# Kernel optimization log

Measured on AMD Instinct MI355X. Metric: run time of the kernel, lower is better.

Reference implementation:

```python
import jax, jax.numpy as jnp
import numpy as np

NUM_CLASSES = 2
THRESHOLD = 0.35   # overlap_thresh
NEG_POS = 7        # negative:positive mining ratio
VAR0, VAR1 = 0.1, 0.2  # self.variance


def point_form(boxes):
    # (cx,cy,w,h) -> (xmin,ymin,xmax,ymax); boxes [P,4]
    return jnp.concatenate([boxes[:, :2] - boxes[:, 2:] / 2,
                            boxes[:, :2] + boxes[:, 2:] / 2], axis=1)


def jaccard(box_a, box_b):
    # box_a [B,O,4] xyxy, box_b [P,4] xyxy -> IoU [B,O,P]
    max_xy = jnp.minimum(box_a[:, :, None, 2:], box_b[None, None, :, 2:])
    min_xy = jnp.maximum(box_a[:, :, None, :2], box_b[None, None, :, :2])
    wh = jnp.clip(max_xy - min_xy, 0.0)
    inter = wh[..., 0] * wh[..., 1]
    area_a = ((box_a[..., 2] - box_a[..., 0]) * (box_a[..., 3] - box_a[..., 1]))[:, :, None]
    area_b = ((box_b[:, 2] - box_b[:, 0]) * (box_b[:, 3] - box_b[:, 1]))[None, None, :]
    return inter / (area_a + area_b - inter)


def encode(matched, priors):
    # matched [B,P,4] xyxy, priors [1,P,4] cxcywh -> offsets [B,P,4]
    g_cxcy = (matched[..., :2] + matched[..., 2:]) / 2 - priors[..., :2]
    g_cxcy = g_cxcy / (VAR0 * priors[..., 2:])
    g_wh = (matched[..., 2:] - matched[..., :2]) / priors[..., 2:]
    g_wh = jnp.log(g_wh) / VAR1
    return jnp.concatenate([g_cxcy, g_wh], axis=-1)


def match(truths, labels, priors):
    # truths [B,O,4] xyxy, labels [B,O] float, priors [P,4] cxcywh
    overlaps = jaccard(truths, point_form(priors))      # [B,O,P]
    best_prior_idx = jnp.argmax(overlaps, axis=2)       # [B,O] best prior per gt
    best_truth_overlap = jnp.max(overlaps, axis=1)      # [B,P]
    best_truth_idx = jnp.argmax(overlaps, axis=1)       # [B,P] best gt per prior
    O = truths.shape[1]

    def fix(bto, bti, bpi):
        # ensure every gt keeps its best prior (index_fill_ / loop in torch)
        bto = bto.at[bpi].set(2.0)
        bti = bti.at[bpi].set(jnp.arange(O))
        return bto, bti

    best_truth_overlap, best_truth_idx = jax.vmap(fix)(
        best_truth_overlap, best_truth_idx, best_prior_idx)
    matched = jnp.take_along_axis(truths, best_truth_idx[..., None], axis=1)  # [B,P,4]
    conf = jnp.take_along_axis(labels, best_truth_idx, axis=1).astype(jnp.int32) + 1
    conf = jnp.where(best_truth_overlap < THRESHOLD, 0, conf)  # background
    loc = encode(matched, priors[None])
    return loc, conf


def setup_inputs() -> dict:
    key = jax.random.key(0)
    k1, k2, k3, k4, k5, k6 = jax.random.split(key, 6)
    B, P, O, C = 32, 32768, 32, NUM_CLASSES
    loc_data = jax.random.normal(k1, (B, P, 4), jnp.float32)
    conf_data = jax.random.normal(k2, (B, P, C), jnp.float32)
    # priors: (cx,cy,w,h) in [0,1], wh in [0.02,0.3]
    p_cxcy = jax.random.uniform(k3, (P, 2), jnp.float32)
    p_wh = 0.02 + 0.28 * jax.random.uniform(k4, (P, 2), jnp.float32)
    priors = jnp.concatenate([p_cxcy, p_wh], axis=1)
    # targets: valid xyxy boxes + label column (label 0 -> class 1 after +1)
    t_cxcy = 0.1 + 0.8 * jax.random.uniform(k5, (B, O, 2), jnp.float32)
    t_wh = 0.05 + 0.2 * jax.random.uniform(k6, (B, O, 2), jnp.float32)
    boxes = jnp.concatenate([t_cxcy - t_wh / 2, t_cxcy + t_wh / 2], axis=2)
    labels = jnp.zeros((B, O, 1), jnp.float32)
    targets = jnp.concatenate([boxes, labels], axis=2)
    return {"loc_data": loc_data, "conf_data": conf_data,
            "priors": priors, "targets": targets}


def reference(loc_data, conf_data, priors, targets):
    B, P, C = conf_data.shape
    truths = targets[..., :4]
    labels = targets[..., 4]
    loc_t, conf_t = match(truths, labels, priors)   # [B,P,4], [B,P] int
    pos = conf_t > 0                                # [B,P]

    # localization: smooth-L1 summed over positives
    diff = loc_data - loc_t
    ad = jnp.abs(diff)
    sl1 = jnp.where(ad < 1.0, 0.5 * diff * diff, ad - 0.5)
    loss_l = jnp.sum(sl1 * pos[..., None].astype(loc_data.dtype))

    # per-prior CE loss for hard-negative mining
    lse = jax.nn.logsumexp(conf_data, axis=2)                            # [B,P]
    picked = jnp.take_along_axis(conf_data, conf_t[..., None], axis=2)[..., 0]
    ce = lse - picked                                                    # [B,P]
    mine = jnp.where(pos, 0.0, ce)
    # double-argsort rank trick (descending)
    loss_idx = jnp.argsort(-mine, axis=1)
    idx_rank = jnp.argsort(loss_idx, axis=1)
    num_pos = jnp.sum(pos, axis=1, keepdims=True)                        # [B,1]
    num_neg = jnp.minimum(NEG_POS * num_pos, P - 1)
    neg = idx_rank < num_neg

    sel = pos | neg
    loss_c = jnp.sum(jnp.where(sel, ce, 0.0))

    N = jnp.maximum(jnp.sum(num_pos).astype(jnp.float32), 1.0)
    return loss_l / N, loss_c / N
```

## Files before the change

### kernel.cpp

```cpp
#include <hip/hip_runtime.h>
#include <stdint.h>

#define NB 32
#define NP 32768
#define NO 32
#define THRESH 0.35f

typedef unsigned long long u64;
typedef unsigned int u32;

__device__ __forceinline__ float iou_corners(float px1, float py1, float px2, float py2, float ab,
                                             float tx1, float ty1, float tx2, float ty2, float aa)
{
#pragma clang fp contract(off)
    float iw = fminf(tx2, px2) - fmaxf(tx1, px1);
    float ih = fminf(ty2, py2) - fmaxf(ty1, py1);
    iw = fmaxf(iw, 0.f); ih = fmaxf(ih, 0.f);
    float inter = iw * ih;
    return __fdividef(inter, aa + ab - inter);
}

__device__ __forceinline__ float smooth_l1_sum(float4 ld, float4 pr, float4 tt)
{
#pragma clang fp contract(off)
    float g0 = __fdividef((tt.x + tt.z) * 0.5f - pr.x, 0.1f * pr.z);
    float g1 = __fdividef((tt.y + tt.w) * 0.5f - pr.y, 0.1f * pr.w);
    float g2 = __logf(__fdividef(tt.z - tt.x, pr.z)) * 5.0f;
    float g3 = __logf(__fdividef(tt.w - tt.y, pr.w)) * 5.0f;
    float d0 = ld.x - g0, d1 = ld.y - g1, d2 = ld.z - g2, d3 = ld.w - g3;
    float a0 = fabsf(d0), a1 = fabsf(d1), a2 = fabsf(d2), a3 = fabsf(d3);
    return (a0 < 1.f ? 0.5f * d0 * d0 : a0 - 0.5f)
         + (a1 < 1.f ? 0.5f * d1 * d1 : a1 - 0.5f)
         + (a2 < 1.f ? 0.5f * d2 * d2 : a2 - 0.5f)
         + (a3 < 1.f ? 0.5f * d3 * d3 : a3 - 0.5f);
}

__device__ __forceinline__ float lse2(float c0, float c1)
{
#pragma clang fp contract(off)
    float mm = fmaxf(c0, c1), mn = fminf(c0, c1);
    return mm + __logf(1.f + __expf(mn - mm));
}

__global__ __launch_bounds__(256) void kern1(
        const float* __restrict__ loc, const float* __restrict__ conf,
        const float* __restrict__ priors, const float* __restrict__ targets,
        float* __restrict__ mine, u64* __restrict__ bpk_part,
        float* __restrict__ part_sl1, float* __restrict__ part_cep, int* __restrict__ part_np,
        float* __restrict__ sl_tot, float* __restrict__ c_tot,
        int* __restrict__ np_tot, int* __restrict__ done_cnt)
{
#pragma clang fp contract(off)
    __shared__ __align__(16) float4 tbc[NO];
    __shared__ float ta[NO], tlab[NO];
    __shared__ u64 keys[NO];
    __shared__ float rs0[4], rs1[4];
    __shared__ int rc[4];
    const int b = blockIdx.y, x = blockIdx.x, tid = threadIdx.x;
    if (b == 0 && x == 0 && tid == 0) {
        *sl_tot = 0.f; *c_tot = 0.f; *np_tot = 0; *done_cnt = 0;
    }
    if (tid < NO * 5) {
        int o = tid / 5, c = tid % 5;
        float v = targets[b * NO * 5 + tid];
        if (c < 4) ((float*)&tbc[o])[c] = v; else tlab[o] = v;
    }
    if (tid < NO) keys[tid] = 0ull;
    __syncthreads();
    if (tid < NO) {
        float4 t = tbc[tid];
        ta[tid] = (t.z - t.x) * (t.w - t.y);
    }
    __syncthreads();

    const int p0 = x * 1024 + tid * 4;
    float4 pr[4];
    float px1[4], py1[4], px2[4], py2[4], ab[4];
#pragma unroll
    for (int j = 0; j < 4; ++j) {
        pr[j] = ((const float4*)priors)[p0 + j];
        px1[j] = pr[j].x - pr[j].z * 0.5f;
        py1[j] = pr[j].y - pr[j].w * 0.5f;
        px2[j] = pr[j].x + pr[j].z * 0.5f;
        py2[j] = pr[j].y + pr[j].w * 0.5f;
        ab[j]  = pr[j].z * pr[j].w;
    }
    u64 bk[4] = {0ull, 0ull, 0ull, 0ull};
    const int lane_o = tid & 31;
    for (int it = 0; it < NO; ++it) {
        const int o = (it + lane_o) & 31;
        float4 tt = tbc[o];
        float aa = ta[o];
        float iou4[4];
#pragma unroll
        for (int j = 0; j < 4; ++j) {
            float iou = iou_corners(px1[j], py1[j], px2[j], py2[j], ab[j],
                                    tt.x, tt.y, tt.z, tt.w, aa);
            iou4[j] = iou;
            u64 ko = ((u64)__float_as_uint(iou) << 6) | (u64)(63 - o);
            bk[j] = bk[j] > ko ? bk[j] : ko;
        }
        float vm = fmaxf(fmaxf(iou4[0], iou4[1]), fmaxf(iou4[2], iou4[3]));
        u64 cur = keys[o];
        if (__float_as_uint(vm) > (u32)(cur >> 32)) {
            float bi = iou4[3]; int bp = p0 + 3;
            if (iou4[2] >= bi) { bi = iou4[2]; bp = p0 + 2; }
            if (iou4[1] >= bi) { bi = iou4[1]; bp = p0 + 1; }
            if (iou4[0] >= bi) { bi = iou4[0]; bp = p0 + 0; }
            atomicMax(&keys[o], ((u64)__float_as_uint(bi) << 32) | (u64)(~(u32)bp));
        }
    }

    const size_t gbase = (size_t)b * NP + p0;
    float4 cfa = ((const float4*)conf)[gbase / 2];
    float4 cfb = ((const float4*)conf)[gbase / 2 + 1];
    float c0[4] = {cfa.x, cfa.z, cfb.x, cfb.z};
    float c1[4] = {cfa.y, cfa.w, cfb.y, cfb.w};
    float4 mout;
    float s_sl1 = 0.f, s_cep = 0.f;
    int np = 0;
#pragma unroll
    for (int j = 0; j < 4; ++j) {
        u32 vb = (u32)(bk[j] >> 6);
        float bv = __uint_as_float(vb);
        int o = 63 - (int)(bk[j] & 63);
        int cf = (bv < THRESH) ? 0 : ((int)tlab[o] + 1);
        bool pos = cf > 0;
        float4 ld = ((const float4*)loc)[gbase + j];
        float sl1 = smooth_l1_sum(ld, pr[j], tbc[o]);
        float ce = lse2(c0[j], c1[j]) - ((cf == 0) ? c0[j] : c1[j]);
        if (pos) { s_sl1 += sl1; s_cep += ce; np++; }
        ((float*)&mout)[j] = pos ? 0.f : ce;
    }
    ((float4*)mine)[gbase / 4] = mout;

#pragma unroll
    for (int m = 32; m; m >>= 1) {
        s_sl1 += __shfl_xor(s_sl1, m, 64);
        s_cep += __shfl_xor(s_cep, m, 64);
        np    += __shfl_xor(np, m, 64);
    }
    int lane = tid & 63, w = tid >> 6;
    if (lane == 0) { rs0[w] = s_sl1; rs1[w] = s_cep; rc[w] = np; }
    __syncthreads();
    if (tid == 0) {
        float t0 = 0.f, t1 = 0.f; int t2 = 0;
        for (int i = 0; i < 4; ++i) { t0 += rs0[i]; t1 += rs1[i]; t2 += rc[i]; }
        part_sl1[b * 32 + x] = t0;
        part_cep[b * 32 + x] = t1;
        part_np [b * 32 + x] = t2;
    }
    if (tid < NO) bpk_part[(b * 32 + x) * 32 + tid] = keys[tid];
}

__global__ __launch_bounds__(1024) void kern3(
        const float* __restrict__ loc, const float* __restrict__ conf,
        const float* __restrict__ priors, const float* __restrict__ targets,
        const u64* __restrict__ bpk_part, const float* __restrict__ mine,
        const float* __restrict__ part_sl1, const float* __restrict__ part_cep,
        const int* __restrict__ part_np,
        float* __restrict__ sl_tot, float* __restrict__ c_tot,
        int* __restrict__ np_tot, int* __restrict__ done_cnt,
        float* __restrict__ out)
{
#pragma clang fp contract(off)
    const int b = blockIdx.x, tid = threadIdx.x;
    const int wave = tid >> 6, lane = tid & 63;
    __shared__ __align__(16) float4 tbc[NO];
    __shared__ float tlab[NO], tas[NO];
    __shared__ u32 pp[NO];
    __shared__ u32 flags[1024];
    __shared__ __align__(16) int hist[16][256];
    __shared__ __align__(16) int total[256];
    __shared__ u32 sh_prefix;
    __shared__ int sh_kk;
    __shared__ float sh_sl1, sh_cep;
    __shared__ int sh_np;
    __shared__ float rs[16];

    if (tid < NO * 5) {
        int o = tid / 5, c = tid % 5;
        float v = targets[b * NO * 5 + tid];
        if (c < 4) ((float*)&tbc[o])[c] = v; else tlab[o] = v;
    }
    flags[tid] = 0u;

    const float* mb = mine + (size_t)b * NP;
    float v[32];
#pragma unroll
    for (int q = 0; q < 8; ++q) {
        float4 t4 = ((const float4*)mb)[q * 1024 + tid];
        v[4 * q] = t4.x; v[4 * q + 1] = t4.y; v[4 * q + 2] = t4.z; v[4 * q + 3] = t4.w;
    }
    __syncthreads();
    if (tid < NO) {
        float4 t = tbc[tid];
        tas[tid] = (t.z - t.x) * (t.w - t.y);
        u64 key = 0ull;
        for (int xx = 0; xx < 32; ++xx) {
            u64 t2 = bpk_part[(b * 32 + xx) * 32 + tid];
            key = t2 > key ? t2 : key;
        }
        pp[tid] = (key >> 32) ? ~(u32)key : 0u;
    }
    __syncthreads();
    if (tid < NO) {
        const int o = tid;
        const u32 p = pp[o];
        float dsl1 = 0.f, dcep = 0.f; int dnp = 0;
        bool last = true;
        for (int o2 = o + 1; o2 < NO; ++o2)
            if (pp[o2] == p) { last = false; break; }
        if (last) {
            float4 prr = ((const float4*)priors)[p];
            float px1 = prr.x - prr.z * 0.5f, py1 = prr.y - prr.w * 0.5f;
            float px2 = prr.x + prr.z * 0.5f, py2 = prr.y + prr.w * 0.5f;
            float ab = prr.z * prr.w;
            float bv = -1.f; int bo_ = 0;
            for (int o2 = 0; o2 < NO; ++o2) {
                float4 t2 = tbc[o2];
                float i2 = iou_corners(px1, py1, px2, py2, ab, t2.x, t2.y, t2.z, t2.w, tas[o2]);
                if (i2 > bv) { bv = i2; bo_ = o2; }
            }
            int cf_pre = (bv < THRESH) ? 0 : ((int)tlab[bo_] + 1);
            size_t gp = (size_t)b * NP + p;
            float4 ld = ((const float4*)loc)[gp];
            float2 c = ((const float2*)conf)[gp];
            float lse = lse2(c.x, c.y);
            int cf_new = (int)tlab[o] + 1;
            dsl1 = smooth_l1_sum(ld, prr, tbc[o]);
            dcep = lse - ((cf_new == 0) ? c.x : c.y);
            dnp = 1;
            if (cf_pre > 0) {
                dsl1 -= smooth_l1_sum(ld, prr, tbc[bo_]);
                dcep -= lse - ((cf_pre == 0) ? c.x : c.y);
                dnp = 0;
            }
            atomicOr(&flags[p >> 5], 1u << (p & 31));
        }
        float a = part_sl1[b * 32 + o] + dsl1;
        float d = part_cep[b * 32 + o] + dcep;
        int   n = part_np [b * 32 + o] + dnp;
#pragma unroll
        for (int m = 16; m; m >>= 1) {
            a += __shfl_xor(a, m, 32);
            d += __shfl_xor(d, m, 32);
            n += __shfl_xor(n, m, 32);
        }
        if (o == 0) {
            sh_sl1 = a; sh_cep = d; sh_np = n;
            sh_prefix = 0u; sh_kk = min(7 * n, NP - 1);
        }
    }
    __syncthreads();
#pragma unroll
    for (int q = 0; q < 8; ++q) {
        u32 word = flags[q * 128 + (tid >> 3)];
#pragma unroll
        for (int c = 0; c < 4; ++c)
            if ((word >> (((tid & 7) << 2) + c)) & 1u) v[4 * q + c] = 0.f;
    }
    const int k = sh_kk;
    float topk = 0.f;
    if (k > 0) {
        int* myh = &hist[wave][0];
        for (int pass = 0; pass < 4; ++pass) {
#pragma unroll
            for (int i = 0; i < 4; ++i) ((int*)hist)[tid + i * 1024] = 0;
            __syncthreads();
            const int shift = 24 - 8 * pass;
            const u32 pfx = sh_prefix;
#pragma unroll 8
            for (int j = 0; j < 32; ++j) {
                u32 kb = __float_as_uint(v[j]);
                if ((u32)(((u64)kb) >> (shift + 8)) == pfx)
                    atomicAdd(&myh[(kb >> shift) & 255], 1);
            }
            __syncthreads();
            if (tid < 256) {
                int s = 0;
#pragma unroll
                for (int w2 = 0; w2 < 16; ++w2) s += hist[w2][tid];
                total[tid] = s;
            }
            __syncthreads();
            if (tid < 64) {
                int4 h4 = ((const int4*)total)[tid];
                int s3 = h4.w, s2 = h4.z + s3, s1 = h4.y + s2, s0 = h4.x + s1;
                int acc = s0;
#pragma unroll
                for (int off = 1; off < 64; off <<= 1) {
                    int u = __shfl_down(acc, off, 64);
                    if (tid + off < 64) acc += u;
                }
                int excl = acc - s0;
                int kk = sh_kk;
                int cand = -1, nkk = 0;
                if (excl + s3 >= kk)      { cand = 4 * tid + 3; nkk = kk - excl; }
                else if (excl + s2 >= kk) { cand = 4 * tid + 2; nkk = kk - excl - s3; }
                else if (excl + s1 >= kk) { cand = 4 * tid + 1; nkk = kk - excl - s2; }
                else if (excl + s0 >= kk) { cand = 4 * tid + 0; nkk = kk - excl - s1; }
                int cmax = cand;
#pragma unroll
                for (int off = 1; off < 64; off <<= 1) cmax = max(cmax, __shfl_xor(cmax, off, 64));
                if (cand >= 0 && cand == cmax) {
                    sh_prefix = (pfx << 8) | (u32)(cand & 255);
                    sh_kk = nkk;
                }
            }
            __syncthreads();
        }
        const u32 T = sh_prefix;
        const float tval = __uint_as_float(T);
        float s = 0.f;
#pragma unroll
        for (int j = 0; j < 32; ++j)
            if (__float_as_uint(v[j]) > T) s += v[j];
#pragma unroll
        for (int m = 32; m; m >>= 1) s += __shfl_xor(s, m, 64);
        if (lane == 0) rs[wave] = s;
        __syncthreads();
        if (tid == 0) {
            float st = 0.f;
            for (int i = 0; i < 16; ++i) st += rs[i];
            topk = st + (float)sh_kk * tval;
        }
    }
    if (tid == 0) {
        atomicAdd(sl_tot, sh_sl1);
        atomicAdd(c_tot, sh_cep + topk);
        atomicAdd(np_tot, sh_np);
        __threadfence();
        int d = atomicAdd(done_cnt, 1);
        if (d == NB - 1) {
            float sl = atomicAdd(sl_tot, 0.f);
            float cc = atomicAdd(c_tot, 0.f);
            int   np = atomicAdd(np_tot, 0);
            float N = fmaxf((float)np, 1.f);
            out[0] = sl / N;
            out[1] = cc / N;
        }
    }
}

extern "C" void kernel_launch(void* const* d_in, const int* in_sizes, int n_in,
                              void* d_out, int out_size, void* d_ws, size_t ws_size,
                              hipStream_t stream) {
    const float* loc     = (const float*)d_in[0];
    const float* conf    = (const float*)d_in[1];
    const float* priors  = (const float*)d_in[2];
    const float* targets = (const float*)d_in[3];
    float* out = (float*)d_out;

    char* ws = (char*)d_ws;
    float* mine     = (float*)ws;
    u64*   bpk_part = (u64*)(ws + 4194304);
    float* part_sl1 = (float*)(ws + 4456448);
    float* part_cep = (float*)(ws + 4460544);
    int*   part_np  = (int*)(ws + 4464640);
    float* sl_tot   = (float*)(ws + 4468736);
    float* c_tot    = (float*)(ws + 4468740);
    int*   np_tot   = (int*)(ws + 4468744);
    int*   done_cnt = (int*)(ws + 4468748);

    dim3 g1(32, NB);
    kern1<<<g1, 256, 0, stream>>>(loc, conf, priors, targets, mine, bpk_part,
                                  part_sl1, part_cep, part_np,
                                  sl_tot, c_tot, np_tot, done_cnt);
    kern3<<<NB, 1024, 0, stream>>>(loc, conf, priors, targets, bpk_part, mine,
                                   part_sl1, part_cep, part_np,
                                   sl_tot, c_tot, np_tot, done_cnt, out);
}
```

Measured before the change: 149.8 us.

## Replace radix-histogram top-k threshold search with bitwise binary search on counts

Replaces the 4-pass 8-bit radix histogram selection for the hard-negative top-k threshold with a binary search over the float bit pattern. Each step counts the elements above the midpoint using register compares and wave shuffles, with one barrier per step, which removes the shared-memory atomics and histogram scans. The cost is up to about 31 iterations, each doing 32 compares plus a block reduction, instead of 4 heavier passes. The search is bounded by the per-block maximum to cut iterations.

```diff
diff --git a/kernel.cpp b/kernel.cpp
--- a/kernel.cpp
+++ b/kernel.cpp
@@ -170,13 +170,11 @@
     __shared__ float tlab[NO], tas[NO];
     __shared__ u32 pp[NO];
     __shared__ u32 flags[1024];
-    __shared__ __align__(16) int hist[16][256];
-    __shared__ __align__(16) int total[256];
-    __shared__ u32 sh_prefix;
-    __shared__ int sh_kk;
+    __shared__ u32 red[2][16];
+    __shared__ float rs[16];
+    __shared__ int rc2[16];
     __shared__ float sh_sl1, sh_cep;
-    __shared__ int sh_np;
-    __shared__ float rs[16];
+    __shared__ int sh_np, sh_k;
 
     if (tid < NO * 5) {
         int o = tid / 5, c = tid % 5;
@@ -249,7 +247,7 @@
         }
         if (o == 0) {
             sh_sl1 = a; sh_cep = d; sh_np = n;
-            sh_prefix = 0u; sh_kk = min(7 * n, NP - 1);
+            sh_k = min(7 * n, NP - 1);
         }
     }
     __syncthreads();
@@ -260,70 +258,59 @@
         for (int c = 0; c < 4; ++c)
             if ((word >> (((tid & 7) << 2) + c)) & 1u) v[4 * q + c] = 0.f;
     }
-    const int k = sh_kk;
+    const int k = sh_k;
     float topk = 0.f;
     if (k > 0) {
-        int* myh = &hist[wave][0];
-        for (int pass = 0; pass < 4; ++pass) {
-#pragma unroll
-            for (int i = 0; i < 4; ++i) ((int*)hist)[tid + i * 1024] = 0;
+        u32 mx = 0;
+#pragma unroll
+        for (int j = 0; j < 32; ++j) mx = max(mx, __float_as_uint(v[j]));
+#pragma unroll
+        for (int m = 32; m; m >>= 1) mx = max(mx, (u32)__shfl_xor((int)mx, m, 64));
+        if (lane == 0) red[0][wave] = mx;
+        __syncthreads();
+        {
+            u32 t = red[0][lane & 15];
+#pragma unroll
+            for (int m = 8; m; m >>= 1) t = max(t, (u32)__shfl_xor((int)t, m, 64));
+            mx = t;
+        }
+        __syncthreads();
+        u32 lo = 0, hi = mx;
+        int parity = 0;
+        while (lo < hi) {
+            u32 mid = lo + ((hi - lo) >> 1);
+            int c = 0;
+#pragma unroll
+            for (int j = 0; j < 32; ++j) c += (__float_as_uint(v[j]) > mid) ? 1 : 0;
+#pragma unroll
+            for (int m = 32; m; m >>= 1) c += __shfl_xor(c, m, 64);
+            if (lane == 0) red[parity][wave] = (u32)c;
             __syncthreads();
-            const int shift = 24 - 8 * pass;
-            const u32 pfx = sh_prefix;
-#pragma unroll 8
-            for (int j = 0; j < 32; ++j) {
-                u32 kb = __float_as_uint(v[j]);
-                if ((u32)(((u64)kb) >> (shift + 8)) == pfx)
-                    atomicAdd(&myh[(kb >> shift) & 255], 1);
-            }
-            __syncthreads();
-            if (tid < 256) {
-                int s = 0;
-#pragma unroll
-                for (int w2 = 0; w2 < 16; ++w2) s += hist[w2][tid];
-                total[tid] = s;
-            }
-            __syncthreads();
-            if (tid < 64) {
-                int4 h4 = ((const int4*)total)[tid];
-                int s3 = h4.w, s2 = h4.z + s3, s1 = h4.y + s2, s0 = h4.x + s1;
-                int acc = s0;
-#pragma unroll
-                for (int off = 1; off < 64; off <<= 1) {
-                    int u = __shfl_down(acc, off, 64);
-                    if (tid + off < 64) acc += u;
-                }
-                int excl = acc - s0;
-                int kk = sh_kk;
-                int cand = -1, nkk = 0;
-                if (excl + s3 >= kk)      { cand = 4 * tid + 3; nkk = kk - excl; }
-                else if (excl + s2 >= kk) { cand = 4 * tid + 2; nkk = kk - excl - s3; }
-                else if (excl + s1 >= kk) { cand = 4 * tid + 1; nkk = kk - excl - s2; }
-                else if (excl + s0 >= kk) { cand = 4 * tid + 0; nkk = kk - excl - s1; }
-                int cmax = cand;
-#pragma unroll
-                for (int off = 1; off < 64; off <<= 1) cmax = max(cmax, __shfl_xor(cmax, off, 64));
-                if (cand >= 0 && cand == cmax) {
-                    sh_prefix = (pfx << 8) | (u32)(cand & 255);
-                    sh_kk = nkk;
-                }
-            }
-            __syncthreads();
-        }
-        const u32 T = sh_prefix;
+            u32 t = red[parity][lane & 15];
+#pragma unroll
+            for (int m = 8; m; m >>= 1) t += (u32)__shfl_xor((int)t, m, 64);
+            if ((int)t < k) hi = mid; else lo = mid + 1;
+            parity ^= 1;
+        }
+        const u32 T = lo;
         const float tval = __uint_as_float(T);
-        float s = 0.f;
-#pragma unroll
-        for (int j = 0; j < 32; ++j)
-            if (__float_as_uint(v[j]) > T) s += v[j];
-#pragma unroll
-        for (int m = 32; m; m >>= 1) s += __shfl_xor(s, m, 64);
-        if (lane == 0) rs[wave] = s;
+        float s = 0.f; int c2 = 0;
+#pragma unroll
+        for (int j = 0; j < 32; ++j) {
+            if (__float_as_uint(v[j]) > T) { s += v[j]; c2++; }
+        }
+#pragma unroll
+        for (int m = 32; m; m >>= 1) {
+            s  += __shfl_xor(s, m, 64);
+            c2 += __shfl_xor(c2, m, 64);
+        }
+        __syncthreads();
+        if (lane == 0) { rs[wave] = s; rc2[wave] = c2; }
         __syncthreads();
         if (tid == 0) {
-            float st = 0.f;
-            for (int i = 0; i < 16; ++i) st += rs[i];
-            topk = st + (float)sh_kk * tval;
+            float st = 0.f; int ct = 0;
+            for (int i = 0; i < 16; ++i) { st += rs[i]; ct += rc2[i]; }
+            topk = st + (float)(k - ct) * tval;
         }
     }
     if (tid == 0) {
```

Result: no change. 149.7 us (-0.1%).
